# Performance work log

Measured on AMD Instinct MI355X. Metric: run time of the kernel, lower is better.

The kernel has to match this reference:

```python
import jax, jax.numpy as jnp
import numpy as np

NEG_INF = -1e30  # stand-in for float('-inf') masked_fill (safe for softmax)


def setup_inputs() -> dict:
    key = jax.random.key(0)
    ks = jax.random.split(key, 7)
    B, T, C, H, D = 4, 2048, 64, 6, 64
    s = 1.0 / np.sqrt(C)
    return {
        "x": jax.random.normal(ks[0], (B, T, C), dtype=jnp.float32),
        "y": jax.random.normal(ks[1], (B, T, C), dtype=jnp.float32),
        "Wq": jax.random.normal(ks[2], (H, C, D), dtype=jnp.float32) * s,
        "Wk": jax.random.normal(ks[3], (H, C, D), dtype=jnp.float32) * s,
        "Wv": jax.random.normal(ks[4], (H, C, D), dtype=jnp.float32) * s,
        "W_proj": jax.random.normal(ks[5], (H * D, C), dtype=jnp.float32) * (1.0 / np.sqrt(H * D)),
        "b_proj": jnp.zeros((C,), dtype=jnp.float32),
    }


def reference(x, y, Wq, Wk, Wv, W_proj, b_proj):
    # x, y: [B, T, C]; per-head projections stacked over H (heads vectorized).
    B, T, C = x.shape
    H, _, D = Wq.shape
    q = jnp.einsum("btc,hcd->bhtd", x, Wq)   # query from decoder input x
    k = jnp.einsum("btc,hcd->bhtd", y, Wk)   # key from encoder output y
    v = jnp.einsum("btc,hcd->bhtd", y, Wv)
    scale = D ** (-0.5)
    wei = jnp.einsum("bhtd,bhsd->bhts", q, k) * scale  # [B,H,T,T]
    # triu(ones(T,T), diagonal=1) future mask (causal)
    future = jnp.triu(jnp.ones((T, T), dtype=bool), k=1)
    wei = jnp.where(future, NEG_INF, wei)
    wei = jax.nn.softmax(wei, axis=-1)  # dropout = identity in eval
    out = jnp.einsum("bhts,bhsd->bhtd", wei, v)          # [B,H,T,D]
    out = out.transpose(0, 2, 1, 3).reshape(B, T, H * D)  # concat heads
    return out @ W_proj + b_proj                          # [B,T,C]
```

## Files before the change

kernel.cpp:

```cpp
#include <hip/hip_runtime.h>


typedef unsigned short u16t;
typedef __attribute__((ext_vector_type(8))) short short8;
typedef __attribute__((ext_vector_type(4))) float float4v;

#define MFMA16(a, b, c) __builtin_amdgcn_mfma_f32_16x16x32_bf16((a), (b), (c), 0, 0, 0)

union U8 { short8 s; unsigned u[4]; };

__device__ __forceinline__ float fexp2(float x) {
  return __builtin_amdgcn_exp2f(x);
}
__device__ __forceinline__ float bf2f(u16t u) {
  return __uint_as_float(((unsigned)u) << 16);
}
__device__ __forceinline__ u16t f2bf(float f) {
  unsigned u = __float_as_uint(f);
  u += 0x7fffu + ((u >> 16) & 1u);
  return (u16t)(u >> 16);
}
__device__ __forceinline__ unsigned bftr(float f) {
  return __float_as_uint(f) >> 16;
}
__device__ __forceinline__ short8 load8_f32_bf16(const float* p) {
  float4 f0 = *(const float4*)p;
  float4 f1 = *(const float4*)(p + 4);
  short8 r;
  r[0] = (short)f2bf(f0.x); r[1] = (short)f2bf(f0.y);
  r[2] = (short)f2bf(f0.z); r[3] = (short)f2bf(f0.w);
  r[4] = (short)f2bf(f1.x); r[5] = (short)f2bf(f1.y);
  r[6] = (short)f2bf(f1.z); r[7] = (short)f2bf(f1.w);
  return r;
}

constexpr int Bb = 4, Tt = 2048, Cc = 64, Hh = 6, Dd = 64;
constexpr int BH = Bb * Hh;
constexpr int NQT = Tt / 64;
constexpr int LDT = 72;
constexpr int LDV = 136;
constexpr int OST = 65;
#define QSCALE (0.125f * 1.44269504088896f)

__global__ __launch_bounds__(256) void prep_kernel(
    const float* __restrict__ Wq, const float* __restrict__ Wk,
    const float* __restrict__ Wv, const float* __restrict__ Wp,
    u16t* __restrict__ Wqt, u16t* __restrict__ Wkt,
    u16t* __restrict__ Wvt, u16t* __restrict__ Wpt) {
  int idx = blockIdx.x * 256 + threadIdx.x;
  {
    int h = idx >> 12, dc = idx & 4095, d = dc >> 6, c = dc & 63;
    int src = h * 4096 + c * 64 + d;
    Wqt[idx] = f2bf(Wq[src]);
    Wkt[idx] = f2bf(Wk[src]);
    Wvt[idx] = f2bf(Wv[src]);
  }
  {
    int c = idx / 384, r = idx - c * 384;
    Wpt[idx] = f2bf(Wp[r * 64 + c]);
  }
}

__global__ __launch_bounds__(256) void qkv_kernel(
    const float* __restrict__ x, const float* __restrict__ y,
    const u16t* __restrict__ Wqt, const u16t* __restrict__ Wkt,
    const u16t* __restrict__ Wvt,
    u16t* __restrict__ Q, u16t* __restrict__ K, u16t* __restrict__ Vt) {
  __shared__ __align__(16) u16t wtq[64 * LDT];
  __shared__ __align__(16) u16t wtk[64 * LDT];
  __shared__ __align__(16) u16t wtv[64 * LDT];

  int bid = blockIdx.x;
  int bh = bid >> 5, tt = bid & 31;
  int b = bh / Hh, h = bh - b * Hh;
  int tid = threadIdx.x;
  int w = tid >> 6, lane = tid & 63;
  int l15 = lane & 15, q4 = lane >> 4;

  {
    const u16t* wq = Wqt + h * 4096;
    const u16t* wk = Wkt + h * 4096;
    const u16t* wv = Wvt + h * 4096;
#pragma unroll
    for (int i = 0; i < 2; ++i) {
      int id = tid * 2 + i;
      int row = id >> 3, c8 = id & 7;
      *(uint4*)&wtq[row * LDT + c8 * 8] = *(const uint4*)(wq + id * 8);
      *(uint4*)&wtk[row * LDT + c8 * 8] = *(const uint4*)(wk + id * 8);
      *(uint4*)&wtv[row * LDT + c8 * 8] = *(const uint4*)(wv + id * 8);
    }
  }

  int trow = tt * 64 + w * 16 + l15;
  const float* xrow = x + ((size_t)b * Tt + trow) * Cc;
  const float* yrow = y + ((size_t)b * Tt + trow) * Cc;
  short8 xa[2], ya[2];
#pragma unroll
  for (int kc = 0; kc < 2; ++kc) {
    xa[kc] = load8_f32_bf16(xrow + kc * 32 + q4 * 8);
    ya[kc] = load8_f32_bf16(yrow + kc * 32 + q4 * 8);
  }
  __syncthreads();

  float4v qa4[4], ka4[4], va4[4];
#pragma unroll
  for (int nc = 0; nc < 4; ++nc) {
    qa4[nc] = (float4v){0.f, 0.f, 0.f, 0.f};
    ka4[nc] = (float4v){0.f, 0.f, 0.f, 0.f};
    va4[nc] = (float4v){0.f, 0.f, 0.f, 0.f};
  }
#pragma unroll
  for (int nc = 0; nc < 4; ++nc) {
#pragma unroll
    for (int kc = 0; kc < 2; ++kc) {
      int off = (nc * 16 + l15) * LDT + kc * 32 + q4 * 8;
      short8 bq = *(const short8*)&wtq[off];
      short8 bk = *(const short8*)&wtk[off];
      short8 bv = *(const short8*)&wtv[off];
      qa4[nc] = MFMA16(xa[kc], bq, qa4[nc]);
      ka4[nc] = MFMA16(ya[kc], bk, ka4[nc]);
      va4[nc] = MFMA16(ya[kc], bv, va4[nc]);
    }
  }
  __syncthreads();

#pragma unroll
  for (int reg = 0; reg < 4; ++reg) {
    int rloc = w * 16 + q4 * 4 + reg;
#pragma unroll
    for (int nc = 0; nc < 4; ++nc) {
      wtq[rloc * LDT + nc * 16 + l15] = f2bf(qa4[nc][reg] * QSCALE);
      wtk[rloc * LDT + nc * 16 + l15] = f2bf(ka4[nc][reg]);
      wtv[(nc * 16 + l15) * LDT + rloc] = f2bf(va4[nc][reg]);
    }
  }
  __syncthreads();

  size_t tilebase = ((size_t)bh * Tt + tt * 64) * Dd;
#pragma unroll
  for (int i = 0; i < 2; ++i) {
    int id = tid * 2 + i;
    int row = id >> 3, c8 = id & 7;
    *(uint4*)&Q[tilebase + row * 64 + c8 * 8] = *(const uint4*)&wtq[row * LDT + c8 * 8];
    *(uint4*)&K[tilebase + row * 64 + c8 * 8] = *(const uint4*)&wtk[row * LDT + c8 * 8];
    *(uint4*)&Vt[((size_t)bh * 64 + row) * Tt + tt * 64 + c8 * 8] =
        *(const uint4*)&wtv[row * LDT + c8 * 8];
  }
}

__global__ __launch_bounds__(256) void attn_kernel(
    const u16t* __restrict__ Q, const u16t* __restrict__ K,
    const u16t* __restrict__ Vt, u16t* __restrict__ att) {
  __shared__ __align__(16) unsigned char smem[128 * LDT * 2 + 64 * LDV * 2];
  u16t* Kl = (u16t*)smem;
  u16t* Vl = (u16t*)(smem + 128 * LDT * 2);
  float* Ol = (float*)smem;
  float* Ll = (float*)(smem + 64 * OST * 4);

  int bid = blockIdx.x;
  int bh = bid % BH;
  int qt = (NQT - 1) - bid / BH;
  int b = bh / Hh, h = bh - (bh / Hh) * Hh;
  int tid = threadIdx.x;
  int w = tid >> 6;
  int lane = tid & 63;
  int l15 = lane & 15, q4 = lane >> 4;

  short8 qf[4][2];
#pragma unroll
  for (int it = 0; it < 4; ++it) {
    const u16t* qb = Q + ((size_t)bh * Tt + qt * 64 + it * 16 + l15) * Dd;
    qf[it][0] = *(const short8*)(qb + q4 * 8);
    qf[it][1] = *(const short8*)(qb + 32 + q4 * 8);
  }

  float4v O[4][4];
#pragma unroll
  for (int it = 0; it < 4; ++it)
#pragma unroll
    for (int nc = 0; nc < 4; ++nc) O[it][nc] = (float4v){0.f, 0.f, 0.f, 0.f};
  float l_[4] = {0.f, 0.f, 0.f, 0.f};

  const u16t* Kbh = K + (size_t)bh * Tt * Dd;
  const u16t* Vbh = Vt + (size_t)bh * Dd * Tt;
  const int bsmax = qt >> 1;

  for (int bs = 0; bs <= bsmax; ++bs) {
    __syncthreads();
    {
      const u16t* ks = Kbh + (size_t)bs * 128 * 64;
      const u16t* vs = Vbh + bs * 128;
#pragma unroll
      for (int i = 0; i < 4; ++i) {
        int id = tid + i * 256;
        *(uint4*)&Kl[(id >> 3) * LDT + (id & 7) * 8] =
            *(const uint4*)(ks + (size_t)(id >> 3) * 64 + (id & 7) * 8);
        *(uint4*)&Vl[(id >> 4) * LDV + (id & 15) * 8] =
            *(const uint4*)(vs + (size_t)(id >> 4) * Tt + (id & 15) * 8);
      }
    }
    __syncthreads();

    bool d0 = (2 * bs == qt);
    bool s1 = (2 * bs + 1 > qt);
    bool d1 = (2 * bs + 1 == qt);

    short8 kf00 = *(const short8*)&Kl[(w * 16 + l15) * LDT + q4 * 8];
    short8 kf01 = *(const short8*)&Kl[(w * 16 + l15) * LDT + 32 + q4 * 8];
    short8 kf10 = kf00, kf11 = kf01;
    if (!s1) {
      kf10 = *(const short8*)&Kl[(64 + w * 16 + l15) * LDT + q4 * 8];
      kf11 = *(const short8*)&Kl[(64 + w * 16 + l15) * LDT + 32 + q4 * 8];
    }
    short8 vf[4];
#pragma unroll
    for (int nc = 0; nc < 4; ++nc) {
      U8 t;
      *(uint2*)&t.u[0] = *(const uint2*)&Vl[(nc * 16 + l15) * LDV + w * 16 + q4 * 4];
      *(uint2*)&t.u[2] = *(const uint2*)&Vl[(nc * 16 + l15) * LDV + 64 + w * 16 + q4 * 4];
      vf[nc] = t.s;
    }

#pragma unroll
    for (int it = 0; it < 4; ++it) {
      if (d0 && w > it) continue;
      float4v S0 = (float4v){0.f, 0.f, 0.f, 0.f};
      S0 = MFMA16(kf00, qf[it][0], S0);
      S0 = MFMA16(kf01, qf[it][1], S0);
      bool m0 = d0 && (w == it);
      float p0[4], p1[4];
#pragma unroll
      for (int reg = 0; reg < 4; ++reg) {
        p0[reg] = (m0 && (q4 * 4 + reg) > l15) ? 0.f : fexp2(S0[reg]);
        l_[it] += p0[reg];
      }
      if (s1 || (d1 && w > it)) {
#pragma unroll
        for (int reg = 0; reg < 4; ++reg) p1[reg] = 0.f;
      } else {
        float4v S1 = (float4v){0.f, 0.f, 0.f, 0.f};
        S1 = MFMA16(kf10, qf[it][0], S1);
        S1 = MFMA16(kf11, qf[it][1], S1);
        bool m1 = d1 && (w == it);
#pragma unroll
        for (int reg = 0; reg < 4; ++reg) {
          p1[reg] = (m1 && (q4 * 4 + reg) > l15) ? 0.f : fexp2(S1[reg]);
          l_[it] += p1[reg];
        }
      }
      U8 pa;
      pa.u[0] = bftr(p0[0]) | (bftr(p0[1]) << 16);
      pa.u[1] = bftr(p0[2]) | (bftr(p0[3]) << 16);
      pa.u[2] = bftr(p1[0]) | (bftr(p1[1]) << 16);
      pa.u[3] = bftr(p1[2]) | (bftr(p1[3]) << 16);
#pragma unroll
      for (int nc = 0; nc < 4; ++nc)
        O[it][nc] = MFMA16(pa.s, vf[nc], O[it][nc]);
    }
  }

#pragma unroll
  for (int it = 0; it < 4; ++it) {
    l_[it] += __shfl_xor(l_[it], 16);
    l_[it] += __shfl_xor(l_[it], 32);
  }

  __syncthreads();
#pragma unroll
  for (int r = 0; r < 4; ++r) {
#pragma unroll
    for (int itc = 0; itc < 4; ++itc) {
      if (((itc - w) & 3) == r) {
#pragma unroll
        for (int nc = 0; nc < 4; ++nc)
#pragma unroll
          for (int reg = 0; reg < 4; ++reg) {
            int addr = (itc * 16 + q4 * 4 + reg) * OST + nc * 16 + l15;
            if (r == 0) Ol[addr] = O[itc][nc][reg];
            else        Ol[addr] += O[itc][nc][reg];
          }
        if (q4 == 0) {
          if (r == 0) Ll[itc * 16 + l15] = l_[itc];
          else        Ll[itc * 16 + l15] += l_[itc];
        }
      }
    }
    __syncthreads();
  }

#pragma unroll
  for (int i = 0; i < 2; ++i) {
    int id = tid * 2 + i;
    int row = id >> 3, c8 = id & 7;
    float inv = 1.0f / Ll[row];
    const float* orow = &Ol[row * OST + c8 * 8];
    U8 o;
#pragma unroll
    for (int k = 0; k < 4; ++k)
      o.u[k] = f2bf(orow[2 * k] * inv) | ((unsigned)f2bf(orow[2 * k + 1] * inv) << 16);
    int t = qt * 64 + row;
    *(uint4*)&att[((size_t)b * Tt + t) * (Hh * Dd) + h * Dd + c8 * 8] = *(const uint4*)&o;
  }
}

constexpr int LDP = 392;

__global__ __launch_bounds__(256) void proj_kernel(
    const u16t* __restrict__ att, const u16t* __restrict__ Wpt,
    const float* __restrict__ bp, float* __restrict__ out) {
  __shared__ __align__(16) u16t wpt[64 * LDP];

  int bid = blockIdx.x;
  int tid = threadIdx.x;
  int w = tid >> 6, lane = tid & 63;
  int l15 = lane & 15, q4 = lane >> 4;

#pragma unroll
  for (int i = 0; i < 12; ++i) {
    int id = tid + i * 256;
    int r = id / 48, c8 = id - r * 48;
    *(uint4*)&wpt[r * LDP + c8 * 8] = *(const uint4*)(Wpt + id * 8);
  }
  __syncthreads();

  int row0 = bid * 64 + w * 16;
  const u16t* arow = att + (size_t)(row0 + l15) * 384;

  float4v acc[4];
#pragma unroll
  for (int nc = 0; nc < 4; ++nc) acc[nc] = (float4v){0.f, 0.f, 0.f, 0.f};

#pragma unroll
  for (int kc = 0; kc < 12; ++kc) {
    short8 a = *(const short8*)(arow + kc * 32 + q4 * 8);
#pragma unroll
    for (int nc = 0; nc < 4; ++nc) {
      short8 bfr = *(const short8*)&wpt[(nc * 16 + l15) * LDP + kc * 32 + q4 * 8];
      acc[nc] = MFMA16(a, bfr, acc[nc]);
    }
  }

  float bv[4];
#pragma unroll
  for (int nc = 0; nc < 4; ++nc) bv[nc] = bp[nc * 16 + l15];
#pragma unroll
  for (int reg = 0; reg < 4; ++reg) {
    int t = row0 + q4 * 4 + reg;
    size_t obase = (size_t)t * 64;
#pragma unroll
    for (int nc = 0; nc < 4; ++nc)
      out[obase + nc * 16 + l15] = acc[nc][reg] + bv[nc];
  }
}

extern "C" void kernel_launch(void* const* d_in, const int* in_sizes, int n_in,
                              void* d_out, int out_size, void* d_ws, size_t ws_size,
                              hipStream_t stream) {
  const float* x  = (const float*)d_in[0];
  const float* y  = (const float*)d_in[1];
  const float* Wq = (const float*)d_in[2];
  const float* Wk = (const float*)d_in[3];
  const float* Wv = (const float*)d_in[4];
  const float* Wp = (const float*)d_in[5];
  const float* bp = (const float*)d_in[6];
  float* out = (float*)d_out;

  const size_t NBH = (size_t)BH * Tt * Dd;
  u16t* Qs   = (u16t*)d_ws;
  u16t* Ks   = Qs + NBH;
  u16t* Vts  = Ks + NBH;
  u16t* attb = Vts + NBH;
  u16t* Wqt  = attb + NBH;
  u16t* Wkt  = Wqt + 24576;
  u16t* Wvt  = Wkt + 24576;
  u16t* Wpt  = Wvt + 24576;

  prep_kernel<<<96, 256, 0, stream>>>(Wq, Wk, Wv, Wp, Wqt, Wkt, Wvt, Wpt);
  qkv_kernel<<<BH * NQT, 256, 0, stream>>>(x, y, Wqt, Wkt, Wvt, Qs, Ks, Vts);
  attn_kernel<<<BH * NQT, 256, 0, stream>>>(Qs, Ks, Vts, attb);
  proj_kernel<<<(Bb * Tt) / 64, 256, 0, stream>>>(attb, Wpt, bp, out);
}
```

Before: 119.9 us.

## Double-buffer K/V tiles via direct global-to-LDS loads with XOR swizzle

The K and V tile staging in the attention loop now uses global_load_lds to copy straight into LDS. It double-buffers across iterations so the next block's load overlaps compute on the current one, with manual vmcnt waits and barriers. Padding is replaced by an XOR-swizzled layout to avoid bank conflicts. LDS use grows to 64KB per block, which may reduce occupancy, and correctness relies on the hand-written waitcnt counts.

Result: no change. 121.6 us (+1.4%).

```diff
diff --git a/kernel.cpp b/kernel.cpp
--- a/kernel.cpp
+++ b/kernel.cpp
@@ -33,12 +33,16 @@
   r[6] = (short)f2bf(f1.z); r[7] = (short)f2bf(f1.w);
   return r;
 }
+__device__ __forceinline__ void ld16(const void* g, void* l) {
+  __builtin_amdgcn_global_load_lds(
+      (const __attribute__((address_space(1))) unsigned int*)g,
+      (__attribute__((address_space(3))) unsigned int*)l, 16, 0, 0);
+}
 
 constexpr int Bb = 4, Tt = 2048, Cc = 64, Hh = 6, Dd = 64;
 constexpr int BH = Bb * Hh;
 constexpr int NQT = Tt / 64;
 constexpr int LDT = 72;
-constexpr int LDV = 136;
 constexpr int OST = 65;
 #define QSCALE (0.125f * 1.44269504088896f)
 
@@ -151,9 +155,7 @@
 __global__ __launch_bounds__(256) void attn_kernel(
     const u16t* __restrict__ Q, const u16t* __restrict__ K,
     const u16t* __restrict__ Vt, u16t* __restrict__ att) {
-  __shared__ __align__(16) unsigned char smem[128 * LDT * 2 + 64 * LDV * 2];
-  u16t* Kl = (u16t*)smem;
-  u16t* Vl = (u16t*)(smem + 128 * LDT * 2);
+  __shared__ __align__(1024) unsigned char smem[2 * 32768];
   float* Ol = (float*)smem;
   float* Ll = (float*)(smem + 64 * OST * 4);
 
@@ -166,6 +168,30 @@
   int lane = tid & 63;
   int l15 = lane & 15, q4 = lane >> 4;
 
+  const u16t* Kbh = K + (size_t)bh * Tt * Dd;
+  const u16t* Vbh = Vt + (size_t)bh * Dd * Tt;
+  const int bsmax = qt >> 1;
+
+  int koff[4], voff[4];
+#pragma unroll
+  for (int s = 0; s < 4; ++s) {
+    int P = (w * 4 + s) * 64 + lane;
+    int kr = P >> 3;
+    koff[s] = kr * 128 + (((P & 7) ^ (kr & 7)) << 4);
+    int vr = P >> 4;
+    voff[s] = vr * (Tt * 2) + (((P & 15) ^ (vr & 7)) << 4);
+  }
+
+  {
+    const unsigned char* ks = (const unsigned char*)Kbh;
+    const unsigned char* vs = (const unsigned char*)Vbh;
+#pragma unroll
+    for (int s = 0; s < 4; ++s) {
+      ld16(ks + koff[s], smem + ((w * 4 + s) << 10));
+      ld16(vs + voff[s], smem + 16384 + ((w * 4 + s) << 10));
+    }
+  }
+
   short8 qf[4][2];
 #pragma unroll
   for (int it = 0; it < 4; ++it) {
@@ -174,6 +200,15 @@
     qf[it][1] = *(const short8*)(qb + 32 + q4 * 8);
   }
 
+  int krow = w * 16 + l15;
+  int ka0 = krow * 128 + ((q4 ^ (krow & 7)) << 4);
+  int va_[4];
+#pragma unroll
+  for (int nc = 0; nc < 4; ++nc) {
+    int vr = nc * 16 + l15;
+    va_[nc] = vr * 256 + (q4 & 1) * 8 + (((w * 2 + (q4 >> 1)) ^ (vr & 7)) << 4);
+  }
+
   float4v O[4][4];
 #pragma unroll
   for (int it = 0; it < 4; ++it)
@@ -181,43 +216,44 @@
     for (int nc = 0; nc < 4; ++nc) O[it][nc] = (float4v){0.f, 0.f, 0.f, 0.f};
   float l_[4] = {0.f, 0.f, 0.f, 0.f};
 
-  const u16t* Kbh = K + (size_t)bh * Tt * Dd;
-  const u16t* Vbh = Vt + (size_t)bh * Dd * Tt;
-  const int bsmax = qt >> 1;
-
   for (int bs = 0; bs <= bsmax; ++bs) {
-    __syncthreads();
-    {
-      const u16t* ks = Kbh + (size_t)bs * 128 * 64;
-      const u16t* vs = Vbh + bs * 128;
-#pragma unroll
-      for (int i = 0; i < 4; ++i) {
-        int id = tid + i * 256;
-        *(uint4*)&Kl[(id >> 3) * LDT + (id & 7) * 8] =
-            *(const uint4*)(ks + (size_t)(id >> 3) * 64 + (id & 7) * 8);
-        *(uint4*)&Vl[(id >> 4) * LDV + (id & 15) * 8] =
-            *(const uint4*)(vs + (size_t)(id >> 4) * Tt + (id & 15) * 8);
+    int cur = bs & 1;
+    unsigned char* Kb = smem + cur * 32768;
+    unsigned char* Vb = Kb + 16384;
+
+    if (bs < bsmax) {
+      unsigned char* Kn = smem + (cur ^ 1) * 32768;
+      const unsigned char* ks = (const unsigned char*)(Kbh + (size_t)(bs + 1) * 128 * 64);
+      const unsigned char* vs = (const unsigned char*)(Vbh + (bs + 1) * 128);
+#pragma unroll
+      for (int s = 0; s < 4; ++s) {
+        ld16(ks + koff[s], Kn + ((w * 4 + s) << 10));
+        ld16(vs + voff[s], Kn + 16384 + ((w * 4 + s) << 10));
       }
-    }
-    __syncthreads();
+      asm volatile("s_waitcnt vmcnt(8)");
+    } else {
+      asm volatile("s_waitcnt vmcnt(0)");
+    }
+    __builtin_amdgcn_s_barrier();
+    __builtin_amdgcn_sched_barrier(0);
 
     bool d0 = (2 * bs == qt);
     bool s1 = (2 * bs + 1 > qt);
     bool d1 = (2 * bs + 1 == qt);
 
-    short8 kf00 = *(const short8*)&Kl[(w * 16 + l15) * LDT + q4 * 8];
-    short8 kf01 = *(const short8*)&Kl[(w * 16 + l15) * LDT + 32 + q4 * 8];
+    short8 kf00 = *(const short8*)(Kb + ka0);
+    short8 kf01 = *(const short8*)(Kb + (ka0 ^ 64));
     short8 kf10 = kf00, kf11 = kf01;
     if (!s1) {
-      kf10 = *(const short8*)&Kl[(64 + w * 16 + l15) * LDT + q4 * 8];
-      kf11 = *(const short8*)&Kl[(64 + w * 16 + l15) * LDT + 32 + q4 * 8];
+      kf10 = *(const short8*)(Kb + 8192 + ka0);
+      kf11 = *(const short8*)(Kb + 8192 + (ka0 ^ 64));
     }
     short8 vf[4];
 #pragma unroll
     for (int nc = 0; nc < 4; ++nc) {
       U8 t;
-      *(uint2*)&t.u[0] = *(const uint2*)&Vl[(nc * 16 + l15) * LDV + w * 16 + q4 * 4];
-      *(uint2*)&t.u[2] = *(const uint2*)&Vl[(nc * 16 + l15) * LDV + 64 + w * 16 + q4 * 4];
+      *(uint2*)&t.u[0] = *(const uint2*)(Vb + va_[nc]);
+      *(uint2*)&t.u[2] = *(const uint2*)(Vb + (va_[nc] ^ 128));
       vf[nc] = t.s;
     }
 
@@ -257,6 +293,10 @@
       for (int nc = 0; nc < 4; ++nc)
         O[it][nc] = MFMA16(pa.s, vf[nc], O[it][nc]);
     }
+
+    __builtin_amdgcn_sched_barrier(0);
+    __builtin_amdgcn_s_barrier();
+    __builtin_amdgcn_sched_barrier(0);
   }
 
 #pragma unroll
```

## Fuse weight prep into consumers, add setprio in attention, split proj tiles

Applied to the files above, without the earlier changes.

Removes the separate prep kernel that transposed and converted the weights to bf16. The qkv and proj kernels now read fp32 weights directly and transpose and convert them into shared memory, which saves one launch and a workspace round trip. The proj kernel now uses 32-row blocks with each wave covering half the output columns, doubling the grid. The attention inner loop is wrapped in s_setprio to favour the MFMA-heavy section. In exchange, the weight conversion is repeated in every block, and the scalar transposed LDS stores may cause bank conflicts.

After: 121.7 us. No clear change (+1.4%).

```diff
diff --git a/kernel.cpp b/kernel.cpp
--- a/kernel.cpp
+++ b/kernel.cpp
@@ -11,9 +11,6 @@
 
 __device__ __forceinline__ float fexp2(float x) {
   return __builtin_amdgcn_exp2f(x);
-}
-__device__ __forceinline__ float bf2f(u16t u) {
-  return __uint_as_float(((unsigned)u) << 16);
 }
 __device__ __forceinline__ u16t f2bf(float f) {
   unsigned u = __float_as_uint(f);
@@ -42,29 +39,10 @@
 constexpr int OST = 65;
 #define QSCALE (0.125f * 1.44269504088896f)
 
-__global__ __launch_bounds__(256) void prep_kernel(
-    const float* __restrict__ Wq, const float* __restrict__ Wk,
-    const float* __restrict__ Wv, const float* __restrict__ Wp,
-    u16t* __restrict__ Wqt, u16t* __restrict__ Wkt,
-    u16t* __restrict__ Wvt, u16t* __restrict__ Wpt) {
-  int idx = blockIdx.x * 256 + threadIdx.x;
-  {
-    int h = idx >> 12, dc = idx & 4095, d = dc >> 6, c = dc & 63;
-    int src = h * 4096 + c * 64 + d;
-    Wqt[idx] = f2bf(Wq[src]);
-    Wkt[idx] = f2bf(Wk[src]);
-    Wvt[idx] = f2bf(Wv[src]);
-  }
-  {
-    int c = idx / 384, r = idx - c * 384;
-    Wpt[idx] = f2bf(Wp[r * 64 + c]);
-  }
-}
-
 __global__ __launch_bounds__(256) void qkv_kernel(
     const float* __restrict__ x, const float* __restrict__ y,
-    const u16t* __restrict__ Wqt, const u16t* __restrict__ Wkt,
-    const u16t* __restrict__ Wvt,
+    const float* __restrict__ Wq, const float* __restrict__ Wk,
+    const float* __restrict__ Wv,
     u16t* __restrict__ Q, u16t* __restrict__ K, u16t* __restrict__ Vt) {
   __shared__ __align__(16) u16t wtq[64 * LDT];
   __shared__ __align__(16) u16t wtk[64 * LDT];
@@ -78,16 +56,22 @@
   int l15 = lane & 15, q4 = lane >> 4;
 
   {
-    const u16t* wq = Wqt + h * 4096;
-    const u16t* wk = Wkt + h * 4096;
-    const u16t* wv = Wvt + h * 4096;
-#pragma unroll
-    for (int i = 0; i < 2; ++i) {
-      int id = tid * 2 + i;
-      int row = id >> 3, c8 = id & 7;
-      *(uint4*)&wtq[row * LDT + c8 * 8] = *(const uint4*)(wq + id * 8);
-      *(uint4*)&wtk[row * LDT + c8 * 8] = *(const uint4*)(wk + id * 8);
-      *(uint4*)&wtv[row * LDT + c8 * 8] = *(const uint4*)(wv + id * 8);
+    const float* wq = Wq + h * 4096 + tid * 16;
+    const float* wk = Wk + h * 4096 + tid * 16;
+    const float* wv = Wv + h * 4096 + tid * 16;
+    int c0 = tid >> 2, d0 = (tid & 3) * 16;
+#pragma unroll
+    for (int j = 0; j < 4; ++j) {
+      float4 fq = *(const float4*)(wq + j * 4);
+      float4 fk = *(const float4*)(wk + j * 4);
+      float4 fv = *(const float4*)(wv + j * 4);
+      int dr = (d0 + j * 4) * LDT + c0;
+      wtq[dr          ] = f2bf(fq.x); wtq[dr + 1 * LDT] = f2bf(fq.y);
+      wtq[dr + 2 * LDT] = f2bf(fq.z); wtq[dr + 3 * LDT] = f2bf(fq.w);
+      wtk[dr          ] = f2bf(fk.x); wtk[dr + 1 * LDT] = f2bf(fk.y);
+      wtk[dr + 2 * LDT] = f2bf(fk.z); wtk[dr + 3 * LDT] = f2bf(fk.w);
+      wtv[dr          ] = f2bf(fv.x); wtv[dr + 1 * LDT] = f2bf(fv.y);
+      wtv[dr + 2 * LDT] = f2bf(fv.z); wtv[dr + 3 * LDT] = f2bf(fv.w);
     }
   }
 
@@ -221,6 +205,7 @@
       vf[nc] = t.s;
     }
 
+    __builtin_amdgcn_s_setprio(1);
 #pragma unroll
     for (int it = 0; it < 4; ++it) {
       if (d0 && w > it) continue;
@@ -257,6 +242,7 @@
       for (int nc = 0; nc < 4; ++nc)
         O[it][nc] = MFMA16(pa.s, vf[nc], O[it][nc]);
     }
+    __builtin_amdgcn_s_setprio(0);
   }
 
 #pragma unroll
@@ -306,7 +292,7 @@
 constexpr int LDP = 392;
 
 __global__ __launch_bounds__(256) void proj_kernel(
-    const u16t* __restrict__ att, const u16t* __restrict__ Wpt,
+    const u16t* __restrict__ att, const float* __restrict__ Wp,
     const float* __restrict__ bp, float* __restrict__ out) {
   __shared__ __align__(16) u16t wpt[64 * LDP];
 
@@ -314,42 +300,47 @@
   int tid = threadIdx.x;
   int w = tid >> 6, lane = tid & 63;
   int l15 = lane & 15, q4 = lane >> 4;
-
-#pragma unroll
-  for (int i = 0; i < 12; ++i) {
-    int id = tid + i * 256;
-    int r = id / 48, c8 = id - r * 48;
-    *(uint4*)&wpt[r * LDP + c8 * 8] = *(const uint4*)(Wpt + id * 8);
-  }
-  __syncthreads();
-
-  int row0 = bid * 64 + w * 16;
+  int rt = w & 1, np = w >> 1;
+
+#pragma unroll
+  for (int i = 0; i < 24; ++i) {
+    int idx = i * 1024 + tid * 4;
+    float4 f = *(const float4*)(Wp + idx);
+    int k = idx >> 6, n0 = idx & 63;
+    int ad = n0 * LDP + k;
+    wpt[ad          ] = f2bf(f.x); wpt[ad + 1 * LDP] = f2bf(f.y);
+    wpt[ad + 2 * LDP] = f2bf(f.z); wpt[ad + 3 * LDP] = f2bf(f.w);
+  }
+  __syncthreads();
+
+  int row0 = bid * 32 + rt * 16;
   const u16t* arow = att + (size_t)(row0 + l15) * 384;
 
-  float4v acc[4];
-#pragma unroll
-  for (int nc = 0; nc < 4; ++nc) acc[nc] = (float4v){0.f, 0.f, 0.f, 0.f};
+  float4v acc[2];
+#pragma unroll
+  for (int j = 0; j < 2; ++j) acc[j] = (float4v){0.f, 0.f, 0.f, 0.f};
 
 #pragma unroll
   for (int kc = 0; kc < 12; ++kc) {
     short8 a = *(const short8*)(arow + kc * 32 + q4 * 8);
 #pragma unroll
-    for (int nc = 0; nc < 4; ++nc) {
+    for (int j = 0; j < 2; ++j) {
+      int nc = np * 2 + j;
       short8 bfr = *(const short8*)&wpt[(nc * 16 + l15) * LDP + kc * 32 + q4 * 8];
-      acc[nc] = MFMA16(a, bfr, acc[nc]);
-    }
-  }
-
-  float bv[4];
-#pragma unroll
-  for (int nc = 0; nc < 4; ++nc) bv[nc] = bp[nc * 16 + l15];
+      acc[j] = MFMA16(a, bfr, acc[j]);
+    }
+  }
+
+  float bv[2];
+#pragma unroll
+  for (int j = 0; j < 2; ++j) bv[j] = bp[(np * 2 + j) * 16 + l15];
 #pragma unroll
   for (int reg = 0; reg < 4; ++reg) {
     int t = row0 + q4 * 4 + reg;
     size_t obase = (size_t)t * 64;
 #pragma unroll
-    for (int nc = 0; nc < 4; ++nc)
-      out[obase + nc * 16 + l15] = acc[nc][reg] + bv[nc];
+    for (int j = 0; j < 2; ++j)
+      out[obase + (np * 2 + j) * 16 + l15] = acc[j][reg] + bv[j];
   }
 }
 
@@ -370,13 +361,8 @@
   u16t* Ks   = Qs + NBH;
   u16t* Vts  = Ks + NBH;
   u16t* attb = Vts + NBH;
-  u16t* Wqt  = attb + NBH;
-  u16t* Wkt  = Wqt + 24576;
-  u16t* Wvt  = Wkt + 24576;
-  u16t* Wpt  = Wvt + 24576;
-
-  prep_kernel<<<96, 256, 0, stream>>>(Wq, Wk, Wv, Wp, Wqt, Wkt, Wvt, Wpt);
-  qkv_kernel<<<BH * NQT, 256, 0, stream>>>(x, y, Wqt, Wkt, Wvt, Qs, Ks, Vts);
+
+  qkv_kernel<<<BH * NQT, 256, 0, stream>>>(x, y, Wq, Wk, Wv, Qs, Ks, Vts);
   attn_kernel<<<BH * NQT, 256, 0, stream>>>(Qs, Ks, Vts, attb);
-  proj_kernel<<<(Bb * Tt) / 64, 256, 0, stream>>>(attb, Wpt, bp, out);
-}
+  proj_kernel<<<(Bb * Tt) / 32, 256, 0, stream>>>(attb, Wp, bp, out);
+}
```
